# Kernel tuning notes

Hardware: AMD Instinct MI355X
Metric: run time of the kernel (lower is better)

## Reference

```python
import jax, jax.numpy as jnp
import numpy as np

N, DIM, K = 262144, 64, 1024

def setup_inputs() -> dict:
    key = jax.random.key(0)
    k1, k2 = jax.random.split(key)
    x = jax.random.normal(k1, (N, DIM), dtype=jnp.float32)
    embed = jax.random.normal(k2, (K, DIM), dtype=jnp.float32)
    return {"x": x, "embed": embed}

def reference(x, embed):
    distances = (jnp.sum(x * x, axis=-1, keepdims=True)
                 - 2.0 * (x @ embed.T)
                 + jnp.sum(embed * embed, axis=-1))  # [N, K]
    idx = jnp.argmin(distances, axis=-1)  # [N]
    # dequantize: embedding lookup
    out = embed[idx]  # [N, DIM]
    return out
```

## Files before the change

kernel.cpp:

```cpp
#include <hip/hip_runtime.h>


#define VQ_N 262144
#define VQ_DIM 64
#define VQ_K 1024
#define NT 64
#define TCH 256
#define FLAG_EPS 1.2e-2f

typedef short short8 __attribute__((ext_vector_type(8)));
typedef float f32x4 __attribute__((ext_vector_type(4)));

#define WS_BFRAG 0
#define WS_E2    (256*1024)
#define WS_FLAGS (260*1024)
#define WS_NEEDED (292*1024)

static __device__ __forceinline__ unsigned short f2bf_rtne(float f) {
    unsigned u = __float_as_uint(f);
    unsigned r = u + 0x7FFFu + ((u >> 16) & 1u);
    return (unsigned short)(r >> 16);
}
static __device__ __forceinline__ float bf2f(unsigned short h) {
    return __uint_as_float(((unsigned)h) << 16);
}

__global__ void vq_prep(const float* __restrict__ embed, unsigned char* ws) {
    int t = blockIdx.x * 256 + threadIdx.x;
    unsigned* flags = (unsigned*)(ws + WS_FLAGS);
    if (t < 8192) flags[t] = 0u;
    if (t < NT * TCH) {
        int ct = t >> 8;
        int c = t & 255;
        int arr = c >> 7;
        int kc = (c >> 6) & 1;
        int l = c & 63;
        int code = ct * 16 + (l & 15);
        int kbase = kc * 32 + ((l >> 4) << 3);
        const float* ep = embed + (size_t)code * VQ_DIM + kbase;
        short8 pack;
#pragma unroll
        for (int j = 0; j < 8; ++j) {
            float v = ep[j];
            unsigned short h = f2bf_rtne(v);
            pack[j] = arr ? (short)f2bf_rtne(v - bf2f(h)) : (short)h;
        }
        ((short8*)(ws + WS_BFRAG))[t] = pack;
    } else if (t < NT * TCH + VQ_K) {
        int code = t - NT * TCH;
        const float* ep = embed + (size_t)code * VQ_DIM;
        float a0 = 0, a1 = 0, a2 = 0, a3 = 0;
#pragma unroll
        for (int j = 0; j < VQ_DIM; j += 4) {
            a0 = fmaf(ep[j], ep[j], a0);
            a1 = fmaf(ep[j + 1], ep[j + 1], a1);
            a2 = fmaf(ep[j + 2], ep[j + 2], a2);
            a3 = fmaf(ep[j + 3], ep[j + 3], a3);
        }
        ((float*)(ws + WS_E2))[code] = (a0 + a1) + (a2 + a3);
    }
}

__global__ __launch_bounds__(256, 4)
void vq_stage1(const float* __restrict__ x, const float* __restrict__ embed,
               unsigned char* ws, float* __restrict__ out) {
    __shared__ int idx_s[128];

    const int tid = threadIdx.x;
    const int lane = tid & 63;
    const int wave = tid >> 6;
    const int gwave = blockIdx.x * 4 + wave;
    const int R0 = gwave * 32;
    const int g = lane >> 4;
    const int khalf = g << 3;

    const short8* bsrc = (const short8*)(ws + WS_BFRAG);
    const float* e2g = (const float*)(ws + WS_E2);
    unsigned* flags = (unsigned*)(ws + WS_FLAGS);

    short8 ah00, ah01, al00, al01, ah10, ah11, al10, al11;
#define MAKE_A(ROW, KC, AH, AL)                                             \
    {                                                                       \
        const float4* p4 = (const float4*)(x + (size_t)(ROW) * VQ_DIM +     \
                                           (KC) * 32 + khalf);              \
        float4 v0 = p4[0], v1 = p4[1];                                      \
        float q0 = -2.0f * v0.x, q1 = -2.0f * v0.y, q2 = -2.0f * v0.z,      \
              q3 = -2.0f * v0.w, q4 = -2.0f * v1.x, q5 = -2.0f * v1.y,      \
              q6 = -2.0f * v1.z, q7 = -2.0f * v1.w;                         \
        unsigned short h0 = f2bf_rtne(q0), h1 = f2bf_rtne(q1),              \
                       h2 = f2bf_rtne(q2), h3 = f2bf_rtne(q3),              \
                       h4 = f2bf_rtne(q4), h5 = f2bf_rtne(q5),              \
                       h6 = f2bf_rtne(q6), h7 = f2bf_rtne(q7);              \
        AH[0] = (short)h0; AH[1] = (short)h1; AH[2] = (short)h2;            \
        AH[3] = (short)h3; AH[4] = (short)h4; AH[5] = (short)h5;            \
        AH[6] = (short)h6; AH[7] = (short)h7;                               \
        AL[0] = (short)f2bf_rtne(q0 - bf2f(h0));                            \
        AL[1] = (short)f2bf_rtne(q1 - bf2f(h1));                            \
        AL[2] = (short)f2bf_rtne(q2 - bf2f(h2));                            \
        AL[3] = (short)f2bf_rtne(q3 - bf2f(h3));                            \
        AL[4] = (short)f2bf_rtne(q4 - bf2f(h4));                            \
        AL[5] = (short)f2bf_rtne(q5 - bf2f(h5));                            \
        AL[6] = (short)f2bf_rtne(q6 - bf2f(h6));                            \
        AL[7] = (short)f2bf_rtne(q7 - bf2f(h7));                            \
    }
    const int row0 = R0 + (lane & 15);
    const int row1 = row0 + 16;
    MAKE_A(row0, 0, ah00, al00)
    MAKE_A(row0, 1, ah01, al01)
    MAKE_A(row1, 0, ah10, al10)
    MAKE_A(row1, 1, ah11, al11)
#undef MAKE_A

    unsigned m1k0[4], m2k0[4], m1k1[4], m2k1[4];
#pragma unroll
    for (int r = 0; r < 4; ++r) {
        m1k0[r] = 0xFFFFFFFFu; m2k0[r] = 0xFFFFFFFFu;
        m1k1[r] = 0xFFFFFFFFu; m2k1[r] = 0xFFFFFFFFu;
    }

#pragma unroll 2
    for (int ct = 0; ct < NT; ++ct) {
        const short8* bt = bsrc + (size_t)ct * TCH;
        short8 bh0 = bt[lane];
        short8 bh1 = bt[64 + lane];
        short8 bl0 = bt[128 + lane];
        short8 bl1 = bt[192 + lane];
        float e2c = e2g[ct * 16 + (lane & 15)] + 256.0f;
        unsigned ctu = (unsigned)ct;

        f32x4 acc0 = {e2c, e2c, e2c, e2c};
        acc0 = __builtin_amdgcn_mfma_f32_16x16x32_bf16(al00, bh0, acc0, 0, 0, 0);
        acc0 = __builtin_amdgcn_mfma_f32_16x16x32_bf16(al01, bh1, acc0, 0, 0, 0);
        acc0 = __builtin_amdgcn_mfma_f32_16x16x32_bf16(ah00, bl0, acc0, 0, 0, 0);
        acc0 = __builtin_amdgcn_mfma_f32_16x16x32_bf16(ah01, bl1, acc0, 0, 0, 0);
        acc0 = __builtin_amdgcn_mfma_f32_16x16x32_bf16(ah00, bh0, acc0, 0, 0, 0);
        acc0 = __builtin_amdgcn_mfma_f32_16x16x32_bf16(ah01, bh1, acc0, 0, 0, 0);

        f32x4 acc1 = {e2c, e2c, e2c, e2c};
        acc1 = __builtin_amdgcn_mfma_f32_16x16x32_bf16(al10, bh0, acc1, 0, 0, 0);
        acc1 = __builtin_amdgcn_mfma_f32_16x16x32_bf16(al11, bh1, acc1, 0, 0, 0);
        acc1 = __builtin_amdgcn_mfma_f32_16x16x32_bf16(ah10, bl0, acc1, 0, 0, 0);
        acc1 = __builtin_amdgcn_mfma_f32_16x16x32_bf16(ah11, bl1, acc1, 0, 0, 0);
        acc1 = __builtin_amdgcn_mfma_f32_16x16x32_bf16(ah10, bh0, acc1, 0, 0, 0);
        acc1 = __builtin_amdgcn_mfma_f32_16x16x32_bf16(ah11, bh1, acc1, 0, 0, 0);

#pragma unroll
        for (int r = 0; r < 4; ++r) {
            unsigned key = (__float_as_uint(acc0[r]) & 0xFFFFFFC0u) | ctu;
            unsigned t1 = m1k0[r] > key ? m1k0[r] : key;
            m2k0[r] = m2k0[r] < t1 ? m2k0[r] : t1;
            m1k0[r] = m1k0[r] < key ? m1k0[r] : key;
        }
#pragma unroll
        for (int r = 0; r < 4; ++r) {
            unsigned key = (__float_as_uint(acc1[r]) & 0xFFFFFFC0u) | ctu;
            unsigned t1 = m1k1[r] > key ? m1k1[r] : key;
            m2k1[r] = m2k1[r] < t1 ? m2k1[r] : t1;
            m1k1[r] = m1k1[r] < key ? m1k1[r] : key;
        }
    }

    unsigned res0[4], res1[4];
#pragma unroll
    for (int r = 0; r < 4; ++r) { res0[r] = (unsigned)(lane & 15); res1[r] = res0[r]; }
#pragma unroll
    for (int m = 1; m <= 8; m <<= 1) {
#pragma unroll
        for (int r = 0; r < 4; ++r) {
            unsigned ok = (unsigned)__shfl_xor((int)m1k0[r], m);
            unsigned ok2 = (unsigned)__shfl_xor((int)m2k0[r], m);
            unsigned orr = (unsigned)__shfl_xor((int)res0[r], m);
            unsigned t1 = m1k0[r] > ok ? m1k0[r] : ok;
            unsigned c2 = ok2 < t1 ? ok2 : t1;
            m2k0[r] = m2k0[r] < c2 ? m2k0[r] : c2;
            bool take = (ok < m1k0[r]) || (ok == m1k0[r] && orr < res0[r]);
            if (take) { m1k0[r] = ok; res0[r] = orr; }
        }
#pragma unroll
        for (int r = 0; r < 4; ++r) {
            unsigned ok = (unsigned)__shfl_xor((int)m1k1[r], m);
            unsigned ok2 = (unsigned)__shfl_xor((int)m2k1[r], m);
            unsigned orr = (unsigned)__shfl_xor((int)res1[r], m);
            unsigned t1 = m1k1[r] > ok ? m1k1[r] : ok;
            unsigned c2 = ok2 < t1 ? ok2 : t1;
            m2k1[r] = m2k1[r] < c2 ? m2k1[r] : c2;
            bool take = (ok < m1k1[r]) || (ok == m1k1[r] && orr < res1[r]);
            if (take) { m1k1[r] = ok; res1[r] = orr; }
        }
    }

    unsigned fmask = 0;
    if ((lane & 15) == 0) {
#pragma unroll
        for (int r = 0; r < 4; ++r) {
            int rl0 = 4 * g + r;
            idx_s[wave * 32 + rl0] = (int)((m1k0[r] & 63u) * 16u + res0[r]);
            float s1 = __uint_as_float(m1k0[r] & 0xFFFFFFC0u);
            float s2 = __uint_as_float(m2k0[r] & 0xFFFFFFC0u);
            if (s2 - s1 < FLAG_EPS) fmask |= 1u << rl0;
            int rl1 = 16 + 4 * g + r;
            idx_s[wave * 32 + rl1] = (int)((m1k1[r] & 63u) * 16u + res1[r]);
            float t1f = __uint_as_float(m1k1[r] & 0xFFFFFFC0u);
            float t2f = __uint_as_float(m2k1[r] & 0xFFFFFFC0u);
            if (t2f - t1f < FLAG_EPS) fmask |= 1u << rl1;
        }
    }
    fmask |= (unsigned)__shfl_xor((int)fmask, 16);
    fmask |= (unsigned)__shfl_xor((int)fmask, 32);
    if (lane == 0) flags[gwave] = fmask;
    __syncthreads();

    const int orow = tid >> 1;
    const int ohalf = tid & 1;
    int code = idx_s[orow];
    const float4* ep = (const float4*)(embed + (size_t)code * VQ_DIM) + ohalf * 8;
    float4* op = (float4*)(out + (size_t)(blockIdx.x * 128 + orow) * VQ_DIM) + ohalf * 8;
#pragma unroll
    for (int j = 0; j < 8; ++j) op[j] = ep[j];
}

__global__ __launch_bounds__(256, 4)
void vq_stage2(const float* __restrict__ x, const float* __restrict__ embed,
               unsigned char* ws, float* __restrict__ out) {
    const unsigned* flags = (const unsigned*)(ws + WS_FLAGS);
    const float* e2 = (const float*)(ws + WS_E2);
    int lane = threadIdx.x & 63;
    int wave = threadIdx.x >> 6;
    int w = blockIdx.x * 4 + wave;
    int rowbase = w * 64;
    unsigned fw = flags[(rowbase >> 5) + (lane >> 5)];
    int bit = (fw >> (lane & 31)) & 1;
    unsigned long long ball = __ballot(bit);
    while (ball) {
        int b = __ffsll(ball) - 1;
        ball &= ball - 1;
        int row = rowbase + b;
        const float* xr = x + (size_t)row * VQ_DIM;
        float best = __builtin_inff();
        int bi = VQ_K;
        for (int t = 0; t < VQ_K / 64; ++t) {
            int c = t * 64 + lane;
            const float* ep = embed + (size_t)c * VQ_DIM;
            float a0 = 0, a1 = 0, a2 = 0, a3 = 0;
#pragma unroll
            for (int j = 0; j < VQ_DIM; j += 4) {
                a0 = fmaf(xr[j], ep[j], a0);
                a1 = fmaf(xr[j + 1], ep[j + 1], a1);
                a2 = fmaf(xr[j + 2], ep[j + 2], a2);
                a3 = fmaf(xr[j + 3], ep[j + 3], a3);
            }
            float dot = (a0 + a1) + (a2 + a3);
            float s = fmaf(-2.0f, dot, e2[c]);
            if (s < best) { best = s; bi = c; }
        }
#pragma unroll
        for (int m = 1; m <= 32; m <<= 1) {
            float ob = __shfl_xor(best, m);
            int oi = __shfl_xor(bi, m);
            if (ob < best || (ob == best && oi < bi)) { best = ob; bi = oi; }
        }
        out[(size_t)row * VQ_DIM + lane] = embed[(size_t)bi * VQ_DIM + lane];
    }
}

__global__ __launch_bounds__(256, 4)
void vq_fallback(const float* __restrict__ x, const float* __restrict__ embed,
                 float* __restrict__ out) {
    __shared__ float e2s[VQ_K];
    const int tid = threadIdx.x;
    for (int c = tid; c < VQ_K; c += 256) {
        const float4* ep = (const float4*)(embed + c * VQ_DIM);
        float s = 0.0f;
#pragma unroll
        for (int j = 0; j < VQ_DIM / 4; ++j) {
            float4 v = ep[j];
            s = fmaf(v.x, v.x, s); s = fmaf(v.y, v.y, s);
            s = fmaf(v.z, v.z, s); s = fmaf(v.w, v.w, s);
        }
        e2s[c] = s;
    }
    __syncthreads();
    const int row = blockIdx.x * 256 + tid;
    float xr[VQ_DIM];
    const float4* xp = (const float4*)(x + (size_t)row * VQ_DIM);
#pragma unroll
    for (int j = 0; j < VQ_DIM / 4; ++j) {
        float4 v = xp[j];
        xr[4 * j] = v.x; xr[4 * j + 1] = v.y; xr[4 * j + 2] = v.z; xr[4 * j + 3] = v.w;
    }
    float best = __builtin_inff();
    int bidx = 0;
    for (int c = 0; c < VQ_K; ++c) {
        const float4* ep = (const float4*)(embed + c * VQ_DIM);
        float a0 = 0, a1 = 0, a2 = 0, a3 = 0;
#pragma unroll
        for (int j = 0; j < VQ_DIM / 4; ++j) {
            float4 v = ep[j];
            a0 = fmaf(xr[4 * j], v.x, a0);
            a1 = fmaf(xr[4 * j + 1], v.y, a1);
            a2 = fmaf(xr[4 * j + 2], v.z, a2);
            a3 = fmaf(xr[4 * j + 3], v.w, a3);
        }
        float score = fmaf(-2.0f, (a0 + a1) + (a2 + a3), e2s[c]);
        if (score < best) { best = score; bidx = c; }
    }
    const float4* bp = (const float4*)(embed + (size_t)bidx * VQ_DIM);
    float4* op = (float4*)(out + (size_t)row * VQ_DIM);
#pragma unroll
    for (int j = 0; j < VQ_DIM / 4; ++j) op[j] = bp[j];
}

extern "C" void kernel_launch(void* const* d_in, const int* in_sizes, int n_in,
                              void* d_out, int out_size, void* d_ws, size_t ws_size,
                              hipStream_t stream) {
    const float* x = (const float*)d_in[0];
    const float* embed = (const float*)d_in[1];
    float* out = (float*)d_out;
    if (ws_size < WS_NEEDED) {
        hipLaunchKernelGGL(vq_fallback, dim3(VQ_N / 256), dim3(256), 0, stream, x, embed, out);
        return;
    }
    unsigned char* ws = (unsigned char*)d_ws;
    hipLaunchKernelGGL(vq_prep, dim3(68), dim3(256), 0, stream, embed, ws);
    hipLaunchKernelGGL(vq_stage1, dim3(VQ_N / 128), dim3(256), 0, stream, x, embed, ws, out);
    hipLaunchKernelGGL(vq_stage2, dim3(VQ_N / 256), dim3(256), 0, stream, x, embed, ws, out);
}
```

Measured before the change: 198.8 us.

## Fuse exact-recheck into stage1 and process 64 rows per wave

Each wave now handles 64 rows instead of 32, so every codebook fragment loaded from the workspace is reused across four MFMA row sets. The separate flag buffer and stage-2 kernel are removed: near-tie rows are rechecked in fp32 inside the same kernel after the output gather, with the x row cached in registers. The output copy is also restructured so each thread writes one float4 per row. This saves a kernel launch and a flag round trip through global memory and halves the B-fragment traffic per row, but raises register pressure (launch bounds drop to 2 blocks per CU) and puts the serial recheck work on the stage-1 critical path.

```diff
diff --git a/kernel.cpp b/kernel.cpp
--- a/kernel.cpp
+++ b/kernel.cpp
@@ -13,8 +13,7 @@
 
 #define WS_BFRAG 0
 #define WS_E2    (256*1024)
-#define WS_FLAGS (260*1024)
-#define WS_NEEDED (292*1024)
+#define WS_NEEDED (260*1024)
 
 static __device__ __forceinline__ unsigned short f2bf_rtne(float f) {
     unsigned u = __float_as_uint(f);
@@ -27,8 +26,6 @@
 
 __global__ void vq_prep(const float* __restrict__ embed, unsigned char* ws) {
     int t = blockIdx.x * 256 + threadIdx.x;
-    unsigned* flags = (unsigned*)(ws + WS_FLAGS);
-    if (t < 8192) flags[t] = 0u;
     if (t < NT * TCH) {
         int ct = t >> 8;
         int c = t & 255;
@@ -61,24 +58,24 @@
     }
 }
 
-__global__ __launch_bounds__(256, 4)
+__global__ __launch_bounds__(256, 2)
 void vq_stage1(const float* __restrict__ x, const float* __restrict__ embed,
                unsigned char* ws, float* __restrict__ out) {
-    __shared__ int idx_s[128];
+    __shared__ int idx_s[4][64];
 
     const int tid = threadIdx.x;
     const int lane = tid & 63;
     const int wave = tid >> 6;
     const int gwave = blockIdx.x * 4 + wave;
-    const int R0 = gwave * 32;
+    const int R0 = gwave * 64;
     const int g = lane >> 4;
     const int khalf = g << 3;
 
     const short8* bsrc = (const short8*)(ws + WS_BFRAG);
     const float* e2g = (const float*)(ws + WS_E2);
-    unsigned* flags = (unsigned*)(ws + WS_FLAGS);
 
     short8 ah00, ah01, al00, al01, ah10, ah11, al10, al11;
+    short8 ah20, ah21, al20, al21, ah30, ah31, al30, al31;
 #define MAKE_A(ROW, KC, AH, AL)                                             \
     {                                                                       \
         const float4* p4 = (const float4*)(x + (size_t)(ROW) * VQ_DIM +     \
@@ -103,19 +100,39 @@
         AL[6] = (short)f2bf_rtne(q6 - bf2f(h6));                            \
         AL[7] = (short)f2bf_rtne(q7 - bf2f(h7));                            \
     }
-    const int row0 = R0 + (lane & 15);
-    const int row1 = row0 + 16;
-    MAKE_A(row0, 0, ah00, al00)
-    MAKE_A(row0, 1, ah01, al01)
-    MAKE_A(row1, 0, ah10, al10)
-    MAKE_A(row1, 1, ah11, al11)
+    const int rowb = R0 + (lane & 15);
+    MAKE_A(rowb +  0, 0, ah00, al00)  MAKE_A(rowb +  0, 1, ah01, al01)
+    MAKE_A(rowb + 16, 0, ah10, al10)  MAKE_A(rowb + 16, 1, ah11, al11)
+    MAKE_A(rowb + 32, 0, ah20, al20)  MAKE_A(rowb + 32, 1, ah21, al21)
+    MAKE_A(rowb + 48, 0, ah30, al30)  MAKE_A(rowb + 48, 1, ah31, al31)
 #undef MAKE_A
 
     unsigned m1k0[4], m2k0[4], m1k1[4], m2k1[4];
+    unsigned m1k2[4], m2k2[4], m1k3[4], m2k3[4];
 #pragma unroll
     for (int r = 0; r < 4; ++r) {
         m1k0[r] = 0xFFFFFFFFu; m2k0[r] = 0xFFFFFFFFu;
         m1k1[r] = 0xFFFFFFFFu; m2k1[r] = 0xFFFFFFFFu;
+        m1k2[r] = 0xFFFFFFFFu; m2k2[r] = 0xFFFFFFFFu;
+        m1k3[r] = 0xFFFFFFFFu; m2k3[r] = 0xFFFFFFFFu;
+    }
+
+#define DO_SET(AH0, AH1, AL0, AL1, M1, M2)                                            \
+    {                                                                                 \
+        f32x4 acc = {e2c, e2c, e2c, e2c};                                             \
+        acc = __builtin_amdgcn_mfma_f32_16x16x32_bf16(AL0, bh0, acc, 0, 0, 0);        \
+        acc = __builtin_amdgcn_mfma_f32_16x16x32_bf16(AL1, bh1, acc, 0, 0, 0);        \
+        acc = __builtin_amdgcn_mfma_f32_16x16x32_bf16(AH0, bl0, acc, 0, 0, 0);        \
+        acc = __builtin_amdgcn_mfma_f32_16x16x32_bf16(AH1, bl1, acc, 0, 0, 0);        \
+        acc = __builtin_amdgcn_mfma_f32_16x16x32_bf16(AH0, bh0, acc, 0, 0, 0);        \
+        acc = __builtin_amdgcn_mfma_f32_16x16x32_bf16(AH1, bh1, acc, 0, 0, 0);        \
+        _Pragma("unroll")                                                             \
+        for (int r = 0; r < 4; ++r) {                                                 \
+            unsigned key = (__float_as_uint(acc[r]) & 0xFFFFFFC0u) | ctu;             \
+            unsigned t1 = M1[r] > key ? M1[r] : key;                                  \
+            M2[r] = M2[r] < t1 ? M2[r] : t1;                                          \
+            M1[r] = M1[r] < key ? M1[r] : key;                                        \
+        }                                                                             \
     }
 
 #pragma unroll 2
@@ -128,114 +145,87 @@
         float e2c = e2g[ct * 16 + (lane & 15)] + 256.0f;
         unsigned ctu = (unsigned)ct;
 
-        f32x4 acc0 = {e2c, e2c, e2c, e2c};
-        acc0 = __builtin_amdgcn_mfma_f32_16x16x32_bf16(al00, bh0, acc0, 0, 0, 0);
-        acc0 = __builtin_amdgcn_mfma_f32_16x16x32_bf16(al01, bh1, acc0, 0, 0, 0);
-        acc0 = __builtin_amdgcn_mfma_f32_16x16x32_bf16(ah00, bl0, acc0, 0, 0, 0);
-        acc0 = __builtin_amdgcn_mfma_f32_16x16x32_bf16(ah01, bl1, acc0, 0, 0, 0);
-        acc0 = __builtin_amdgcn_mfma_f32_16x16x32_bf16(ah00, bh0, acc0, 0, 0, 0);
-        acc0 = __builtin_amdgcn_mfma_f32_16x16x32_bf16(ah01, bh1, acc0, 0, 0, 0);
-
-        f32x4 acc1 = {e2c, e2c, e2c, e2c};
-        acc1 = __builtin_amdgcn_mfma_f32_16x16x32_bf16(al10, bh0, acc1, 0, 0, 0);
-        acc1 = __builtin_amdgcn_mfma_f32_16x16x32_bf16(al11, bh1, acc1, 0, 0, 0);
-        acc1 = __builtin_amdgcn_mfma_f32_16x16x32_bf16(ah10, bl0, acc1, 0, 0, 0);
-        acc1 = __builtin_amdgcn_mfma_f32_16x16x32_bf16(ah11, bl1, acc1, 0, 0, 0);
-        acc1 = __builtin_amdgcn_mfma_f32_16x16x32_bf16(ah10, bh0, acc1, 0, 0, 0);
-        acc1 = __builtin_amdgcn_mfma_f32_16x16x32_bf16(ah11, bh1, acc1, 0, 0, 0);
-
-#pragma unroll
-        for (int r = 0; r < 4; ++r) {
-            unsigned key = (__float_as_uint(acc0[r]) & 0xFFFFFFC0u) | ctu;
-            unsigned t1 = m1k0[r] > key ? m1k0[r] : key;
-            m2k0[r] = m2k0[r] < t1 ? m2k0[r] : t1;
-            m1k0[r] = m1k0[r] < key ? m1k0[r] : key;
-        }
-#pragma unroll
-        for (int r = 0; r < 4; ++r) {
-            unsigned key = (__float_as_uint(acc1[r]) & 0xFFFFFFC0u) | ctu;
-            unsigned t1 = m1k1[r] > key ? m1k1[r] : key;
-            m2k1[r] = m2k1[r] < t1 ? m2k1[r] : t1;
-            m1k1[r] = m1k1[r] < key ? m1k1[r] : key;
-        }
-    }
-
-    unsigned res0[4], res1[4];
-#pragma unroll
-    for (int r = 0; r < 4; ++r) { res0[r] = (unsigned)(lane & 15); res1[r] = res0[r]; }
+        DO_SET(ah00, ah01, al00, al01, m1k0, m2k0)
+        DO_SET(ah10, ah11, al10, al11, m1k1, m2k1)
+        DO_SET(ah20, ah21, al20, al21, m1k2, m2k2)
+        DO_SET(ah30, ah31, al30, al31, m1k3, m2k3)
+    }
+#undef DO_SET
+
+    unsigned res0[4], res1[4], res2[4], res3[4];
+#pragma unroll
+    for (int r = 0; r < 4; ++r) {
+        res0[r] = (unsigned)(lane & 15); res1[r] = res0[r];
+        res2[r] = res0[r]; res3[r] = res0[r];
+    }
+#define RED_STEP(M1, M2, RES, m)                                                      \
+    {                                                                                 \
+        _Pragma("unroll")                                                             \
+        for (int r = 0; r < 4; ++r) {                                                 \
+            unsigned ok = (unsigned)__shfl_xor((int)M1[r], m);                        \
+            unsigned ok2 = (unsigned)__shfl_xor((int)M2[r], m);                       \
+            unsigned orr = (unsigned)__shfl_xor((int)RES[r], m);                      \
+            unsigned t1 = M1[r] > ok ? M1[r] : ok;                                    \
+            unsigned c2 = ok2 < t1 ? ok2 : t1;                                        \
+            M2[r] = M2[r] < c2 ? M2[r] : c2;                                          \
+            bool take = (ok < M1[r]) || (ok == M1[r] && orr < RES[r]);                \
+            if (take) { M1[r] = ok; RES[r] = orr; }                                   \
+        }                                                                             \
+    }
 #pragma unroll
     for (int m = 1; m <= 8; m <<= 1) {
-#pragma unroll
-        for (int r = 0; r < 4; ++r) {
-            unsigned ok = (unsigned)__shfl_xor((int)m1k0[r], m);
-            unsigned ok2 = (unsigned)__shfl_xor((int)m2k0[r], m);
-            unsigned orr = (unsigned)__shfl_xor((int)res0[r], m);
-            unsigned t1 = m1k0[r] > ok ? m1k0[r] : ok;
-            unsigned c2 = ok2 < t1 ? ok2 : t1;
-            m2k0[r] = m2k0[r] < c2 ? m2k0[r] : c2;
-            bool take = (ok < m1k0[r]) || (ok == m1k0[r] && orr < res0[r]);
-            if (take) { m1k0[r] = ok; res0[r] = orr; }
-        }
-#pragma unroll
-        for (int r = 0; r < 4; ++r) {
-            unsigned ok = (unsigned)__shfl_xor((int)m1k1[r], m);
-            unsigned ok2 = (unsigned)__shfl_xor((int)m2k1[r], m);
-            unsigned orr = (unsigned)__shfl_xor((int)res1[r], m);
-            unsigned t1 = m1k1[r] > ok ? m1k1[r] : ok;
-            unsigned c2 = ok2 < t1 ? ok2 : t1;
-            m2k1[r] = m2k1[r] < c2 ? m2k1[r] : c2;
-            bool take = (ok < m1k1[r]) || (ok == m1k1[r] && orr < res1[r]);
-            if (take) { m1k1[r] = ok; res1[r] = orr; }
-        }
-    }
-
-    unsigned fmask = 0;
+        RED_STEP(m1k0, m2k0, res0, m)
+        RED_STEP(m1k1, m2k1, res1, m)
+        RED_STEP(m1k2, m2k2, res2, m)
+        RED_STEP(m1k3, m2k3, res3, m)
+    }
+#undef RED_STEP
+
+    unsigned long long lmask = 0ull;
     if ((lane & 15) == 0) {
-#pragma unroll
-        for (int r = 0; r < 4; ++r) {
-            int rl0 = 4 * g + r;
-            idx_s[wave * 32 + rl0] = (int)((m1k0[r] & 63u) * 16u + res0[r]);
-            float s1 = __uint_as_float(m1k0[r] & 0xFFFFFFC0u);
-            float s2 = __uint_as_float(m2k0[r] & 0xFFFFFFC0u);
-            if (s2 - s1 < FLAG_EPS) fmask |= 1u << rl0;
-            int rl1 = 16 + 4 * g + r;
-            idx_s[wave * 32 + rl1] = (int)((m1k1[r] & 63u) * 16u + res1[r]);
-            float t1f = __uint_as_float(m1k1[r] & 0xFFFFFFC0u);
-            float t2f = __uint_as_float(m2k1[r] & 0xFFFFFFC0u);
-            if (t2f - t1f < FLAG_EPS) fmask |= 1u << rl1;
-        }
-    }
-    fmask |= (unsigned)__shfl_xor((int)fmask, 16);
-    fmask |= (unsigned)__shfl_xor((int)fmask, 32);
-    if (lane == 0) flags[gwave] = fmask;
+#define PUB(M1, M2, RES, SET)                                                         \
+        _Pragma("unroll")                                                             \
+        for (int r = 0; r < 4; ++r) {                                                 \
+            int p = (SET) * 16 + 4 * g + r;                                           \
+            idx_s[wave][p] = (int)((M1[r] & 63u) * 16u + RES[r]);                     \
+            float s1 = __uint_as_float(M1[r] & 0xFFFFFFC0u);                          \
+            float s2 = __uint_as_float(M2[r] & 0xFFFFFFC0u);                          \
+            if (s2 - s1 < FLAG_EPS) lmask |= 1ull << p;                               \
+        }
+        PUB(m1k0, m2k0, res0, 0)
+        PUB(m1k1, m2k1, res1, 1)
+        PUB(m1k2, m2k2, res2, 2)
+        PUB(m1k3, m2k3, res3, 3)
+#undef PUB
+    }
+    lmask |= (unsigned long long)__shfl_xor((long long)lmask, 16);
+    lmask |= (unsigned long long)__shfl_xor((long long)lmask, 32);
+    unsigned long long wmask = (unsigned long long)__shfl((long long)lmask, 0);
     __syncthreads();
 
-    const int orow = tid >> 1;
-    const int ohalf = tid & 1;
-    int code = idx_s[orow];
-    const float4* ep = (const float4*)(embed + (size_t)code * VQ_DIM) + ohalf * 8;
-    float4* op = (float4*)(out + (size_t)(blockIdx.x * 128 + orow) * VQ_DIM) + ohalf * 8;
-#pragma unroll
-    for (int j = 0; j < 8; ++j) op[j] = ep[j];
-}
-
-__global__ __launch_bounds__(256, 4)
-void vq_stage2(const float* __restrict__ x, const float* __restrict__ embed,
-               unsigned char* ws, float* __restrict__ out) {
-    const unsigned* flags = (const unsigned*)(ws + WS_FLAGS);
-    const float* e2 = (const float*)(ws + WS_E2);
-    int lane = threadIdx.x & 63;
-    int wave = threadIdx.x >> 6;
-    int w = blockIdx.x * 4 + wave;
-    int rowbase = w * 64;
-    unsigned fw = flags[(rowbase >> 5) + (lane >> 5)];
-    int bit = (fw >> (lane & 31)) & 1;
-    unsigned long long ball = __ballot(bit);
-    while (ball) {
-        int b = __ffsll(ball) - 1;
-        ball &= ball - 1;
-        int row = rowbase + b;
+    const int chunk = tid & 15;
+#pragma unroll
+    for (int jj = 0; jj < 16; ++jj) {
+        int rib = jj * 16 + (tid >> 4);
+        int code = idx_s[rib >> 6][rib & 63];
+        const float4* ep = (const float4*)(embed + (size_t)code * VQ_DIM) + chunk;
+        float4* op = (float4*)(out + (size_t)(blockIdx.x * 256 + rib) * VQ_DIM) + chunk;
+        *op = *ep;
+    }
+    __syncthreads();
+
+    while (wmask) {
+        int b = __ffsll((unsigned long long)wmask) - 1;
+        wmask &= wmask - 1;
+        int row = R0 + b;
         const float* xr = x + (size_t)row * VQ_DIM;
+        float xv[VQ_DIM];
+#pragma unroll
+        for (int j = 0; j < VQ_DIM / 4; ++j) {
+            float4 v = ((const float4*)xr)[j];
+            xv[4 * j] = v.x; xv[4 * j + 1] = v.y;
+            xv[4 * j + 2] = v.z; xv[4 * j + 3] = v.w;
+        }
         float best = __builtin_inff();
         int bi = VQ_K;
         for (int t = 0; t < VQ_K / 64; ++t) {
@@ -244,14 +234,14 @@
             float a0 = 0, a1 = 0, a2 = 0, a3 = 0;
 #pragma unroll
             for (int j = 0; j < VQ_DIM; j += 4) {
-                a0 = fmaf(xr[j], ep[j], a0);
-                a1 = fmaf(xr[j + 1], ep[j + 1], a1);
-                a2 = fmaf(xr[j + 2], ep[j + 2], a2);
-                a3 = fmaf(xr[j + 3], ep[j + 3], a3);
+                a0 = fmaf(xv[j], ep[j], a0);
+                a1 = fmaf(xv[j + 1], ep[j + 1], a1);
+                a2 = fmaf(xv[j + 2], ep[j + 2], a2);
+                a3 = fmaf(xv[j + 3], ep[j + 3], a3);
             }
             float dot = (a0 + a1) + (a2 + a3);
-            float s = fmaf(-2.0f, dot, e2[c]);
-            if (s < best) { best = s; bi = c; }
+            float s = fmaf(-2.0f, dot, e2g[c]);
+            if (s < best || (s == best && c < bi)) { best = s; bi = c; }
         }
 #pragma unroll
         for (int m = 1; m <= 32; m <<= 1) {
@@ -322,6 +312,5 @@
     }
     unsigned char* ws = (unsigned char*)d_ws;
     hipLaunchKernelGGL(vq_prep, dim3(68), dim3(256), 0, stream, embed, ws);
-    hipLaunchKernelGGL(vq_stage1, dim3(VQ_N / 128), dim3(256), 0, stream, x, embed, ws, out);
-    hipLaunchKernelGGL(vq_stage2, dim3(VQ_N / 256), dim3(256), 0, stream, x, embed, ws, out);
-}
+    hipLaunchKernelGGL(vq_stage1, dim3(VQ_N / 256), dim3(256), 0, stream, x, embed, ws, out);
+}
```

Measured after the change: 183.3 us. 7.8% less time.

## Switch split-precision MFMA from bf16 to scaled fp16 with exact float argmin tracking

Applied to the files above, without the earlier changes.

Replaces the bf16 hi/lo split with an fp16 hi plus a lo residual scaled by 4096, which gives a much more accurate three-term product. The two correction terms accumulate in a separate accumulator and are rescaled by fma, so the main and correction MFMA chains can interleave. The argmin now tracks full float values and a code index instead of keys with truncated mantissas, which allows a far tighter ambiguity threshold (1.5e-3). The point is to flag fewer rows for the slow fp32 recheck in stage2. The cost is extra VALU work per tile and more registers, and fp16 could overflow on inputs larger than the test data.

```diff
diff --git a/kernel.cpp b/kernel.cpp
--- a/kernel.cpp
+++ b/kernel.cpp
@@ -6,24 +6,17 @@
 #define VQ_K 1024
 #define NT 64
 #define TCH 256
-#define FLAG_EPS 1.2e-2f
-
-typedef short short8 __attribute__((ext_vector_type(8)));
+#define FLAG_EPS 1.5e-3f
+#define LO_SCALE 4096.0f
+#define LO_INV   2.44140625e-4f
+
+typedef _Float16 half8 __attribute__((ext_vector_type(8)));
 typedef float f32x4 __attribute__((ext_vector_type(4)));
 
 #define WS_BFRAG 0
 #define WS_E2    (256*1024)
 #define WS_FLAGS (260*1024)
 #define WS_NEEDED (292*1024)
-
-static __device__ __forceinline__ unsigned short f2bf_rtne(float f) {
-    unsigned u = __float_as_uint(f);
-    unsigned r = u + 0x7FFFu + ((u >> 16) & 1u);
-    return (unsigned short)(r >> 16);
-}
-static __device__ __forceinline__ float bf2f(unsigned short h) {
-    return __uint_as_float(((unsigned)h) << 16);
-}
 
 __global__ void vq_prep(const float* __restrict__ embed, unsigned char* ws) {
     int t = blockIdx.x * 256 + threadIdx.x;
@@ -38,14 +31,18 @@
         int code = ct * 16 + (l & 15);
         int kbase = kc * 32 + ((l >> 4) << 3);
         const float* ep = embed + (size_t)code * VQ_DIM + kbase;
-        short8 pack;
+        half8 pack;
 #pragma unroll
         for (int j = 0; j < 8; ++j) {
             float v = ep[j];
-            unsigned short h = f2bf_rtne(v);
-            pack[j] = arr ? (short)f2bf_rtne(v - bf2f(h)) : (short)h;
-        }
-        ((short8*)(ws + WS_BFRAG))[t] = pack;
+            _Float16 h = (_Float16)v;
+            if (arr) {
+                pack[j] = (_Float16)((v - (float)h) * LO_SCALE);
+            } else {
+                pack[j] = h;
+            }
+        }
+        ((half8*)(ws + WS_BFRAG))[t] = pack;
     } else if (t < NT * TCH + VQ_K) {
         int code = t - NT * TCH;
         const float* ep = embed + (size_t)code * VQ_DIM;
@@ -64,7 +61,7 @@
 __global__ __launch_bounds__(256, 4)
 void vq_stage1(const float* __restrict__ x, const float* __restrict__ embed,
                unsigned char* ws, float* __restrict__ out) {
-    __shared__ int idx_s[128];
+    __shared__ int idx_s[4][32];
 
     const int tid = threadIdx.x;
     const int lane = tid & 63;
@@ -72,13 +69,14 @@
     const int gwave = blockIdx.x * 4 + wave;
     const int R0 = gwave * 32;
     const int g = lane >> 4;
+    const int res = lane & 15;
     const int khalf = g << 3;
 
-    const short8* bsrc = (const short8*)(ws + WS_BFRAG);
+    const half8* bsrc = (const half8*)(ws + WS_BFRAG);
     const float* e2g = (const float*)(ws + WS_E2);
     unsigned* flags = (unsigned*)(ws + WS_FLAGS);
 
-    short8 ah00, ah01, al00, al01, ah10, ah11, al10, al11;
+    half8 ah00, ah01, al00, al01, ah10, ah11, al10, al11;
 #define MAKE_A(ROW, KC, AH, AL)                                             \
     {                                                                       \
         const float4* p4 = (const float4*)(x + (size_t)(ROW) * VQ_DIM +     \
@@ -87,23 +85,21 @@
         float q0 = -2.0f * v0.x, q1 = -2.0f * v0.y, q2 = -2.0f * v0.z,      \
               q3 = -2.0f * v0.w, q4 = -2.0f * v1.x, q5 = -2.0f * v1.y,      \
               q6 = -2.0f * v1.z, q7 = -2.0f * v1.w;                         \
-        unsigned short h0 = f2bf_rtne(q0), h1 = f2bf_rtne(q1),              \
-                       h2 = f2bf_rtne(q2), h3 = f2bf_rtne(q3),              \
-                       h4 = f2bf_rtne(q4), h5 = f2bf_rtne(q5),              \
-                       h6 = f2bf_rtne(q6), h7 = f2bf_rtne(q7);              \
-        AH[0] = (short)h0; AH[1] = (short)h1; AH[2] = (short)h2;            \
-        AH[3] = (short)h3; AH[4] = (short)h4; AH[5] = (short)h5;            \
-        AH[6] = (short)h6; AH[7] = (short)h7;                               \
-        AL[0] = (short)f2bf_rtne(q0 - bf2f(h0));                            \
-        AL[1] = (short)f2bf_rtne(q1 - bf2f(h1));                            \
-        AL[2] = (short)f2bf_rtne(q2 - bf2f(h2));                            \
-        AL[3] = (short)f2bf_rtne(q3 - bf2f(h3));                            \
-        AL[4] = (short)f2bf_rtne(q4 - bf2f(h4));                            \
-        AL[5] = (short)f2bf_rtne(q5 - bf2f(h5));                            \
-        AL[6] = (short)f2bf_rtne(q6 - bf2f(h6));                            \
-        AL[7] = (short)f2bf_rtne(q7 - bf2f(h7));                            \
-    }
-    const int row0 = R0 + (lane & 15);
+        _Float16 h0 = (_Float16)q0, h1 = (_Float16)q1, h2 = (_Float16)q2,   \
+                 h3 = (_Float16)q3, h4 = (_Float16)q4, h5 = (_Float16)q5,   \
+                 h6 = (_Float16)q6, h7 = (_Float16)q7;                      \
+        AH[0] = h0; AH[1] = h1; AH[2] = h2; AH[3] = h3;                     \
+        AH[4] = h4; AH[5] = h5; AH[6] = h6; AH[7] = h7;                     \
+        AL[0] = (_Float16)((q0 - (float)h0) * LO_SCALE);                    \
+        AL[1] = (_Float16)((q1 - (float)h1) * LO_SCALE);                    \
+        AL[2] = (_Float16)((q2 - (float)h2) * LO_SCALE);                    \
+        AL[3] = (_Float16)((q3 - (float)h3) * LO_SCALE);                    \
+        AL[4] = (_Float16)((q4 - (float)h4) * LO_SCALE);                    \
+        AL[5] = (_Float16)((q5 - (float)h5) * LO_SCALE);                    \
+        AL[6] = (_Float16)((q6 - (float)h6) * LO_SCALE);                    \
+        AL[7] = (_Float16)((q7 - (float)h7) * LO_SCALE);                    \
+    }
+    const int row0 = R0 + res;
     const int row1 = row0 + 16;
     MAKE_A(row0, 0, ah00, al00)
     MAKE_A(row0, 1, ah01, al01)
@@ -111,98 +107,100 @@
     MAKE_A(row1, 1, ah11, al11)
 #undef MAKE_A
 
-    unsigned m1k0[4], m2k0[4], m1k1[4], m2k1[4];
+    const f32x4 zero4 = {0.0f, 0.0f, 0.0f, 0.0f};
+    float m1v0[4], m2v0[4], m1v1[4], m2v1[4];
+    unsigned m1c0[4], m1c1[4];
 #pragma unroll
     for (int r = 0; r < 4; ++r) {
-        m1k0[r] = 0xFFFFFFFFu; m2k0[r] = 0xFFFFFFFFu;
-        m1k1[r] = 0xFFFFFFFFu; m2k1[r] = 0xFFFFFFFFu;
+        m1v0[r] = __builtin_inff(); m2v0[r] = __builtin_inff(); m1c0[r] = 0u;
+        m1v1[r] = __builtin_inff(); m2v1[r] = __builtin_inff(); m1c1[r] = 0u;
     }
 
 #pragma unroll 2
     for (int ct = 0; ct < NT; ++ct) {
-        const short8* bt = bsrc + (size_t)ct * TCH;
-        short8 bh0 = bt[lane];
-        short8 bh1 = bt[64 + lane];
-        short8 bl0 = bt[128 + lane];
-        short8 bl1 = bt[192 + lane];
-        float e2c = e2g[ct * 16 + (lane & 15)] + 256.0f;
+        const half8* bt = bsrc + (size_t)ct * TCH;
+        half8 bh0 = bt[lane];
+        half8 bh1 = bt[64 + lane];
+        half8 bl0 = bt[128 + lane];
+        half8 bl1 = bt[192 + lane];
+        float e2c = e2g[ct * 16 + res];
         unsigned ctu = (unsigned)ct;
 
-        f32x4 acc0 = {e2c, e2c, e2c, e2c};
-        acc0 = __builtin_amdgcn_mfma_f32_16x16x32_bf16(al00, bh0, acc0, 0, 0, 0);
-        acc0 = __builtin_amdgcn_mfma_f32_16x16x32_bf16(al01, bh1, acc0, 0, 0, 0);
-        acc0 = __builtin_amdgcn_mfma_f32_16x16x32_bf16(ah00, bl0, acc0, 0, 0, 0);
-        acc0 = __builtin_amdgcn_mfma_f32_16x16x32_bf16(ah01, bl1, acc0, 0, 0, 0);
-        acc0 = __builtin_amdgcn_mfma_f32_16x16x32_bf16(ah00, bh0, acc0, 0, 0, 0);
-        acc0 = __builtin_amdgcn_mfma_f32_16x16x32_bf16(ah01, bh1, acc0, 0, 0, 0);
-
-        f32x4 acc1 = {e2c, e2c, e2c, e2c};
-        acc1 = __builtin_amdgcn_mfma_f32_16x16x32_bf16(al10, bh0, acc1, 0, 0, 0);
-        acc1 = __builtin_amdgcn_mfma_f32_16x16x32_bf16(al11, bh1, acc1, 0, 0, 0);
-        acc1 = __builtin_amdgcn_mfma_f32_16x16x32_bf16(ah10, bl0, acc1, 0, 0, 0);
-        acc1 = __builtin_amdgcn_mfma_f32_16x16x32_bf16(ah11, bl1, acc1, 0, 0, 0);
-        acc1 = __builtin_amdgcn_mfma_f32_16x16x32_bf16(ah10, bh0, acc1, 0, 0, 0);
-        acc1 = __builtin_amdgcn_mfma_f32_16x16x32_bf16(ah11, bh1, acc1, 0, 0, 0);
+        f32x4 am0 = {e2c, e2c, e2c, e2c};
+        f32x4 ac0;
+        ac0 = __builtin_amdgcn_mfma_f32_16x16x32_f16(al00, bh0, zero4, 0, 0, 0);
+        am0 = __builtin_amdgcn_mfma_f32_16x16x32_f16(ah00, bh0, am0, 0, 0, 0);
+        ac0 = __builtin_amdgcn_mfma_f32_16x16x32_f16(al01, bh1, ac0, 0, 0, 0);
+        am0 = __builtin_amdgcn_mfma_f32_16x16x32_f16(ah01, bh1, am0, 0, 0, 0);
+        ac0 = __builtin_amdgcn_mfma_f32_16x16x32_f16(ah00, bl0, ac0, 0, 0, 0);
+        ac0 = __builtin_amdgcn_mfma_f32_16x16x32_f16(ah01, bl1, ac0, 0, 0, 0);
+
+        f32x4 am1 = {e2c, e2c, e2c, e2c};
+        f32x4 ac1;
+        ac1 = __builtin_amdgcn_mfma_f32_16x16x32_f16(al10, bh0, zero4, 0, 0, 0);
+        am1 = __builtin_amdgcn_mfma_f32_16x16x32_f16(ah10, bh0, am1, 0, 0, 0);
+        ac1 = __builtin_amdgcn_mfma_f32_16x16x32_f16(al11, bh1, ac1, 0, 0, 0);
+        am1 = __builtin_amdgcn_mfma_f32_16x16x32_f16(ah11, bh1, am1, 0, 0, 0);
+        ac1 = __builtin_amdgcn_mfma_f32_16x16x32_f16(ah10, bl0, ac1, 0, 0, 0);
+        ac1 = __builtin_amdgcn_mfma_f32_16x16x32_f16(ah11, bl1, ac1, 0, 0, 0);
 
 #pragma unroll
         for (int r = 0; r < 4; ++r) {
-            unsigned key = (__float_as_uint(acc0[r]) & 0xFFFFFFC0u) | ctu;
-            unsigned t1 = m1k0[r] > key ? m1k0[r] : key;
-            m2k0[r] = m2k0[r] < t1 ? m2k0[r] : t1;
-            m1k0[r] = m1k0[r] < key ? m1k0[r] : key;
+            float s = fmaf(ac0[r], LO_INV, am0[r]);
+            bool c = s < m1v0[r];
+            float mx = fmaxf(m1v0[r], s);
+            m2v0[r] = fminf(m2v0[r], mx);
+            m1v0[r] = fminf(m1v0[r], s);
+            m1c0[r] = c ? ctu : m1c0[r];
         }
 #pragma unroll
         for (int r = 0; r < 4; ++r) {
-            unsigned key = (__float_as_uint(acc1[r]) & 0xFFFFFFC0u) | ctu;
-            unsigned t1 = m1k1[r] > key ? m1k1[r] : key;
-            m2k1[r] = m2k1[r] < t1 ? m2k1[r] : t1;
-            m1k1[r] = m1k1[r] < key ? m1k1[r] : key;
-        }
-    }
-
-    unsigned res0[4], res1[4];
-#pragma unroll
-    for (int r = 0; r < 4; ++r) { res0[r] = (unsigned)(lane & 15); res1[r] = res0[r]; }
+            float s = fmaf(ac1[r], LO_INV, am1[r]);
+            bool c = s < m1v1[r];
+            float mx = fmaxf(m1v1[r], s);
+            m2v1[r] = fminf(m2v1[r], mx);
+            m1v1[r] = fminf(m1v1[r], s);
+            m1c1[r] = c ? ctu : m1c1[r];
+        }
+    }
+
+    int code0[4], code1[4];
+#pragma unroll
+    for (int r = 0; r < 4; ++r) {
+        code0[r] = (int)(m1c0[r] * 16u) + res;
+        code1[r] = (int)(m1c1[r] * 16u) + res;
+    }
+#define RED_STEP(MV, M2, CODE, m)                                                     \
+    {                                                                                 \
+        _Pragma("unroll")                                                             \
+        for (int r = 0; r < 4; ++r) {                                                 \
+            float ov = __shfl_xor(MV[r], m);                                          \
+            float om2 = __shfl_xor(M2[r], m);                                         \
+            int oc = __shfl_xor(CODE[r], m);                                          \
+            float mx = fmaxf(MV[r], ov);                                              \
+            float c2 = fminf(om2, mx);                                                \
+            M2[r] = fminf(M2[r], c2);                                                 \
+            bool take = (ov < MV[r]) || (ov == MV[r] && oc < CODE[r]);                \
+            if (take) { MV[r] = ov; CODE[r] = oc; }                                   \
+        }                                                                             \
+    }
 #pragma unroll
     for (int m = 1; m <= 8; m <<= 1) {
-#pragma unroll
-        for (int r = 0; r < 4; ++r) {
-            unsigned ok = (unsigned)__shfl_xor((int)m1k0[r], m);
-            unsigned ok2 = (unsigned)__shfl_xor((int)m2k0[r], m);
-            unsigned orr = (unsigned)__shfl_xor((int)res0[r], m);
-            unsigned t1 = m1k0[r] > ok ? m1k0[r] : ok;
-            unsigned c2 = ok2 < t1 ? ok2 : t1;
-            m2k0[r] = m2k0[r] < c2 ? m2k0[r] : c2;
-            bool take = (ok < m1k0[r]) || (ok == m1k0[r] && orr < res0[r]);
-            if (take) { m1k0[r] = ok; res0[r] = orr; }
-        }
-#pragma unroll
-        for (int r = 0; r < 4; ++r) {
-            unsigned ok = (unsigned)__shfl_xor((int)m1k1[r], m);
-            unsigned ok2 = (unsigned)__shfl_xor((int)m2k1[r], m);
-            unsigned orr = (unsigned)__shfl_xor((int)res1[r], m);
-            unsigned t1 = m1k1[r] > ok ? m1k1[r] : ok;
-            unsigned c2 = ok2 < t1 ? ok2 : t1;
-            m2k1[r] = m2k1[r] < c2 ? m2k1[r] : c2;
-            bool take = (ok < m1k1[r]) || (ok == m1k1[r] && orr < res1[r]);
-            if (take) { m1k1[r] = ok; res1[r] = orr; }
-        }
-    }
+        RED_STEP(m1v0, m2v0, code0, m)
+        RED_STEP(m1v1, m2v1, code1, m)
+    }
+#undef RED_STEP
 
     unsigned fmask = 0;
-    if ((lane & 15) == 0) {
+    if (res == 0) {
 #pragma unroll
         for (int r = 0; r < 4; ++r) {
             int rl0 = 4 * g + r;
-            idx_s[wave * 32 + rl0] = (int)((m1k0[r] & 63u) * 16u + res0[r]);
-            float s1 = __uint_as_float(m1k0[r] & 0xFFFFFFC0u);
-            float s2 = __uint_as_float(m2k0[r] & 0xFFFFFFC0u);
-            if (s2 - s1 < FLAG_EPS) fmask |= 1u << rl0;
+            idx_s[wave][rl0] = code0[r];
+            if (m2v0[r] - m1v0[r] < FLAG_EPS) fmask |= 1u << rl0;
             int rl1 = 16 + 4 * g + r;
-            idx_s[wave * 32 + rl1] = (int)((m1k1[r] & 63u) * 16u + res1[r]);
-            float t1f = __uint_as_float(m1k1[r] & 0xFFFFFFC0u);
-            float t2f = __uint_as_float(m2k1[r] & 0xFFFFFFC0u);
-            if (t2f - t1f < FLAG_EPS) fmask |= 1u << rl1;
+            idx_s[wave][rl1] = code1[r];
+            if (m2v1[r] - m1v1[r] < FLAG_EPS) fmask |= 1u << rl1;
         }
     }
     fmask |= (unsigned)__shfl_xor((int)fmask, 16);
@@ -212,7 +210,7 @@
 
     const int orow = tid >> 1;
     const int ohalf = tid & 1;
-    int code = idx_s[orow];
+    int code = idx_s[orow >> 5][orow & 31];
     const float4* ep = (const float4*)(embed + (size_t)code * VQ_DIM) + ohalf * 8;
     float4* op = (float4*)(out + (size_t)(blockIdx.x * 128 + orow) * VQ_DIM) + ohalf * 8;
 #pragma unroll
@@ -251,7 +249,7 @@
             }
             float dot = (a0 + a1) + (a2 + a3);
             float s = fmaf(-2.0f, dot, e2[c]);
-            if (s < best) { best = s; bi = c; }
+            if (s < best || (s == best && c < bi)) { best = s; bi = c; }
         }
 #pragma unroll
         for (int m = 1; m <= 32; m <<= 1) {
```

New measurement: 182.8 us. 8.0% less time.
